# Kernel optimization log

Hardware: AMD Instinct MI355X
Metric: run time of the kernel (lower is better)

The kernel has to match this reference:

```python
import jax, jax.numpy as jnp
import numpy as np

B, T, C, H, W = 16, 32, 64, 16, 16
NUM_FEAT = 10


def setup_inputs() -> dict:
    key = jax.random.key(0)
    ks = jax.random.split(key, 8)
    CHW = C * H * W
    G = NUM_FEAT * H * W
    init = lambda k, shape, fan: jax.random.normal(k, shape, jnp.float32) / np.sqrt(fan).astype(np.float32)
    return {
        "input": jax.random.normal(ks[0], (B, T, C, H, W), jnp.float32),
        "input1": jax.random.normal(ks[1], (B, T, C, H, W), jnp.float32),  # unused by forward
        "act_weights": jax.random.uniform(ks[2], (3,), jnp.float32),
        "conv1_w": init(ks[3], (NUM_FEAT, CHW), CHW),   # Conv1d kernel_size=1 -> plain matmul weight
        "conv1_b": jnp.zeros((NUM_FEAT,), jnp.float32),
        "G3_w": init(ks[4], (G, CHW), CHW),
        "G3_b": jnp.zeros((G,), jnp.float32),
        "ffnn1_w": init(ks[5], (T, T), T),              # torch Linear weight [out,in]
        "ffnn1_b": jnp.zeros((T,), jnp.float32),
    }


def reference(input, input1, act_weights, conv1_w, conv1_b, G3_w, G3_b, ffnn1_w, ffnn1_b):
    Bb, Tt, Cc, Hh, Ww = input.shape
    x = input.reshape(Bb, Tt, Cc * Hh * Ww)                       # [B,T,CHW] (== transposed conv1d input)
    # conv1 (1x1 conv) -> [B,T,F]; AvgPool1d(num_feat) over feature dim -> [B,T]
    f = jnp.einsum('btc,fc->btf', x, conv1_w) + conv1_b
    pooled = f.mean(axis=-1)                                      # [B,T]
    # ffnn1: Linear(T,T): y = pooled @ W^T + b
    z = jnp.einsum('bt,st->bs', pooled, ffnn1_w) + ffnn1_b        # [B,T]
    # G3 (1x1 conv) -> [B,T,G] with G = num_feat*H*W (original permutes to [B,T,G])
    g = jnp.einsum('btc,gc->btg', x, G3_w) + G3_b
    # diag_embed(act(z)) @ g is exactly a per-(b,t) elementwise scale of g.
    gates = (act_weights[0] * jax.nn.relu(z)
             + act_weights[1] * jax.nn.sigmoid(z)
             + act_weights[2] * jax.nn.softmax(z, axis=1))        # softmax over T (dim=1)
    out = (gates[:, :, None] * g).reshape(Bb, Tt, NUM_FEAT, Hh, Ww)
    return out
```

## Files before the change

### kernel.cpp

```cpp
#include <hip/hip_runtime.h>
#include <hip/hip_bf16.h>

#define K_DIM 16384
#define M_DIM 512
#define N_DIM 2560
#define BM 256
#define BN 160
#define BK 64
#define KSPLIT 8
#define KCH (K_DIM / KSPLIT)
#define NT (KCH / BK)

typedef float f32x4 __attribute__((ext_vector_type(4)));
typedef __bf16 bf16x8 __attribute__((ext_vector_type(8)));

__device__ __forceinline__ unsigned short f2bf(float f){
  union { float f; unsigned u; } v; v.f = f;
  unsigned r = v.u + 0x7FFFu + ((v.u >> 16) & 1u);
  return (unsigned short)(r >> 16);
}
__device__ __forceinline__ unsigned bfpack2(float lo, float hi){
  return (unsigned)f2bf(lo) | ((unsigned)f2bf(hi) << 16);
}

__global__ __launch_bounds__(256)
void prep_kernel(const float* __restrict__ conv1_w, const float* __restrict__ conv1_b,
                 float* __restrict__ w_mean, float* __restrict__ b_mean)
{
  int c = blockIdx.x * 256 + threadIdx.x;
  if (c < K_DIM){
    float s = 0.f;
    #pragma unroll
    for (int f = 0; f < 10; ++f) s += conv1_w[f * K_DIM + c];
    w_mean[c] = s * 0.1f;
  }
  if (blockIdx.x == 0 && threadIdx.x == 0){
    float s = 0.f;
    #pragma unroll
    for (int f = 0; f < 10; ++f) s += conv1_b[f];
    *b_mean = s * 0.1f;
  }
}

__global__ __launch_bounds__(256)
void pooled_kernel(const float* __restrict__ X, const float* __restrict__ w_mean,
                   const float* __restrict__ b_mean, float* __restrict__ pooled,
                   unsigned short* __restrict__ xbf)
{
  const int row = blockIdx.x;
  const int tid = threadIdx.x;
  const float* xr = X + (size_t)row * K_DIM;
  unsigned short* xb = xbf + (size_t)row * K_DIM;
  float s = 0.f;
  #pragma unroll 2
  for (int i = 0; i < 8; ++i){
    int idx = (tid + 256 * i) * 8;
    float4 a0 = *(const float4*)(xr + idx);
    float4 a1 = *(const float4*)(xr + idx + 4);
    float4 w0 = *(const float4*)(w_mean + idx);
    float4 w1 = *(const float4*)(w_mean + idx + 4);
    s += a0.x*w0.x + a0.y*w0.y + a0.z*w0.z + a0.w*w0.w
       + a1.x*w1.x + a1.y*w1.y + a1.z*w1.z + a1.w*w1.w;
    uint4 p;
    p.x = bfpack2(a0.x, a0.y); p.y = bfpack2(a0.z, a0.w);
    p.z = bfpack2(a1.x, a1.y); p.w = bfpack2(a1.z, a1.w);
    *(uint4*)(xb + idx) = p;
  }
  #pragma unroll
  for (int off = 32; off; off >>= 1) s += __shfl_down(s, off);
  __shared__ float red[4];
  if ((tid & 63) == 0) red[tid >> 6] = s;
  __syncthreads();
  if (tid == 0) pooled[row] = red[0] + red[1] + red[2] + red[3] + *b_mean;
}

__global__ __launch_bounds__(512)
void gates_kernel(const float* __restrict__ pooled, const float* __restrict__ fw,
                  const float* __restrict__ fb, const float* __restrict__ aw,
                  float* __restrict__ gates)
{
  __shared__ float ps[512];
  int tid = threadIdx.x;
  ps[tid] = pooled[tid];
  __syncthreads();
  int b = tid >> 5, s = tid & 31;
  float z = fb[s];
  #pragma unroll
  for (int t = 0; t < 32; ++t) z += ps[b * 32 + t] * fw[s * 32 + t];
  float mx = z;
  #pragma unroll
  for (int off = 16; off; off >>= 1) mx = fmaxf(mx, __shfl_xor(mx, off));
  float e = expf(z - mx);
  float sum = e;
  #pragma unroll
  for (int off = 16; off; off >>= 1) sum += __shfl_xor(sum, off);
  float sm = e / sum;
  float relu = z > 0.f ? z : 0.f;
  float sig = 1.f / (1.f + expf(-z));
  gates[tid] = aw[0] * relu + aw[1] * sig + aw[2] * sm;
}

__global__ __launch_bounds__(512, 2)
void gemm_kernel(const unsigned short* __restrict__ Abf, const float* __restrict__ W,
                 float* __restrict__ outp, int mode)
{
  __shared__ __align__(16) char smem[106496];
  char* bufA0 = smem;
  char* bufA1 = smem + 32768;
  char* bufB0 = smem + 65536;
  char* bufB1 = smem + 86016;

  const int tid  = threadIdx.x;
  const int lane = tid & 63;
  const int wv   = tid >> 6;
  const int wm   = (wv >> 1) * 64;
  const int wn   = (wv & 1) * 80;

  const int id = blockIdx.x;
  const int kz = id & 7;
  const int r  = id >> 3;
  const int m0 = (r & 1) * BM;
  const int n0 = (r >> 1) * BN;
  const int kbase = kz * KCH;

  f32x4 acc[4][5] = {};

  const int arow0 = tid >> 3;
  const int ac8   = (tid & 7) ^ (arow0 & 7);
  const unsigned short* asrc = Abf + (size_t)(m0 + arow0) * K_DIM + ac8 * 8;
  const int adst = tid * 16;

  auto stageA = [&](char* dst, int k0){
    #pragma unroll
    for (int j = 0; j < 4; ++j){
      __builtin_amdgcn_global_load_lds(
        (const __attribute__((address_space(1))) void*)(asrc + (size_t)j * 64 * K_DIM + k0),
        (__attribute__((address_space(3))) void*)(dst + j * 8192 + adst),
        16, 0, 0);
    }
  };

  const float* bsrcs[5];
  int boff[5];
  #pragma unroll
  for (int j = 0; j < 5; ++j){
    int u = j * 512 + tid;
    int brow = u >> 4;
    int bc4  = u & 15;
    bsrcs[j] = W + (size_t)(n0 + brow) * K_DIM + kbase + bc4 * 4;
    boff[j]  = brow * 128 + ((bc4 * 8) ^ ((brow & 7) << 4));
  }

  auto loadB = [&](int kt, float4* rr){
    #pragma unroll
    for (int j = 0; j < 5; ++j) rr[j] = *(const float4*)(bsrcs[j] + kt * BK);
  };
  auto writeB = [&](char* dst, const float4* rr){
    #pragma unroll
    for (int j = 0; j < 5; ++j){
      uint2 u;
      u.x = bfpack2(rr[j].x, rr[j].y);
      u.y = bfpack2(rr[j].z, rr[j].w);
      *(uint2*)(dst + boff[j]) = u;
    }
  };

  auto compute = [&](const char* A_, const char* B_){
    #pragma unroll
    for (int kk = 0; kk < 2; ++kk){
      bf16x8 af[4], bfv[5];
      const int kbyte = kk * 64 + (lane >> 4) * 16;
      #pragma unroll
      for (int i = 0; i < 4; ++i){
        int row = wm + i * 16 + (lane & 15);
        af[i] = *(const bf16x8*)(A_ + row * 128 + (kbyte ^ ((row & 7) << 4)));
      }
      #pragma unroll
      for (int j = 0; j < 5; ++j){
        int rowb = wn + j * 16 + (lane & 15);
        bfv[j] = *(const bf16x8*)(B_ + rowb * 128 + (kbyte ^ ((rowb & 7) << 4)));
      }
      #pragma unroll
      for (int i = 0; i < 4; ++i)
        #pragma unroll
        for (int j = 0; j < 5; ++j)
          acc[i][j] = __builtin_amdgcn_mfma_f32_16x16x32_bf16(af[i], bfv[j], acc[i][j], 0, 0, 0);
    }
  };

  float4 rbC[5], rbN[5];
  loadB(0, rbC);
  writeB(bufB0, rbC);
  loadB(1, rbC);
  stageA(bufA0, kbase);
  __syncthreads();

  #define BODY(T, RC, RN)                                       \
    do {                                                        \
      char* An = ((T) & 1) ? bufA0 : bufA1;                     \
      char* Ac = ((T) & 1) ? bufA1 : bufA0;                     \
      char* Bc = ((T) & 1) ? bufB1 : bufB0;                     \
      char* Bn = ((T) & 1) ? bufB0 : bufB1;                     \
      if ((T) + 1 < NT) stageA(An, kbase + ((T) + 1) * BK);     \
      if ((T) + 2 < NT) loadB((T) + 2, RN);                     \
      compute(Ac, Bc);                                          \
      __syncthreads();                                          \
      if ((T) + 1 < NT) writeB(Bn, RC);                         \
      __syncthreads();                                          \
    } while (0)

  for (int t = 0; t < NT; t += 2){
    BODY(t, rbC, rbN);
    BODY(t + 1, rbN, rbC);
  }
  #undef BODY

  if (mode == 0){
    float* P = outp + (size_t)kz * M_DIM * N_DIM;
    #pragma unroll
    for (int i = 0; i < 4; ++i){
      int rbase = m0 + wm + i * 16 + (lane >> 4) * 4;
      #pragma unroll
      for (int j = 0; j < 5; ++j){
        int col = n0 + wn + j * 16 + (lane & 15);
        #pragma unroll
        for (int r2 = 0; r2 < 4; ++r2)
          P[(size_t)(rbase + r2) * N_DIM + col] = acc[i][j][r2];
      }
    }
  } else {
    #pragma unroll
    for (int i = 0; i < 4; ++i){
      int rbase = m0 + wm + i * 16 + (lane >> 4) * 4;
      #pragma unroll
      for (int j = 0; j < 5; ++j){
        int col = n0 + wn + j * 16 + (lane & 15);
        #pragma unroll
        for (int r2 = 0; r2 < 4; ++r2)
          atomicAdd(&outp[(size_t)(rbase + r2) * N_DIM + col], acc[i][j][r2]);
      }
    }
  }
}

__global__ __launch_bounds__(256)
void reduce_kernel(const float* __restrict__ part, const float* __restrict__ gates,
                   const float* __restrict__ bias, float* __restrict__ out, int ksplit)
{
  int i4 = blockIdx.x * 256 + threadIdx.x;
  if (i4 >= M_DIM * N_DIM / 4) return;
  size_t off = (size_t)i4 * 4;
  int m = (int)(off / N_DIM);
  int n = (int)(off % N_DIM);
  float sx = 0.f, sy = 0.f, sz = 0.f, sw = 0.f;
  for (int z = 0; z < ksplit; ++z){
    float4 p = *(const float4*)(part + (size_t)z * M_DIM * N_DIM + off);
    sx += p.x; sy += p.y; sz += p.z; sw += p.w;
  }
  float4 bv = *(const float4*)(bias + n);
  float g = gates[m];
  float4 o;
  o.x = g * (sx + bv.x); o.y = g * (sy + bv.y);
  o.z = g * (sz + bv.z); o.w = g * (sw + bv.w);
  *(float4*)(out + off) = o;
}

__global__ __launch_bounds__(256)
void finalize_kernel(float* __restrict__ out, const float* __restrict__ gates,
                     const float* __restrict__ bias)
{
  int i4 = blockIdx.x * 256 + threadIdx.x;
  if (i4 >= M_DIM * N_DIM / 4) return;
  size_t off = (size_t)i4 * 4;
  int m = (int)(off / N_DIM);
  int n = (int)(off % N_DIM);
  float4 o = *(const float4*)(out + off);
  float4 bv = *(const float4*)(bias + n);
  float g = gates[m];
  o.x = g * (o.x + bv.x); o.y = g * (o.y + bv.y);
  o.z = g * (o.z + bv.z); o.w = g * (o.w + bv.w);
  *(float4*)(out + off) = o;
}

extern "C" void kernel_launch(void* const* d_in, const int* in_sizes, int n_in,
                              void* d_out, int out_size, void* d_ws, size_t ws_size,
                              hipStream_t stream)
{
  const float* input   = (const float*)d_in[0];
  const float* aw      = (const float*)d_in[2];
  const float* conv1_w = (const float*)d_in[3];
  const float* conv1_b = (const float*)d_in[4];
  const float* G3_w    = (const float*)d_in[5];
  const float* G3_b    = (const float*)d_in[6];
  const float* ffnn1_w = (const float*)d_in[7];
  const float* ffnn1_b = (const float*)d_in[8];
  float* out = (float*)d_out;

  float* wsf    = (float*)d_ws;
  float* w_mean = wsf;
  float* pooled = wsf + 16384;
  float* gates  = wsf + 16896;
  float* b_mean = wsf + 17408;
  unsigned short* xbf = (unsigned short*)(wsf + 17472);
  float* partial = wsf + 17472 + (size_t)M_DIM * K_DIM / 2;

  const size_t need_det = ((size_t)17472 + (size_t)M_DIM * K_DIM / 2
                           + (size_t)KSPLIT * M_DIM * N_DIM) * 4;

  prep_kernel<<<64, 256, 0, stream>>>(conv1_w, conv1_b, w_mean, b_mean);
  pooled_kernel<<<512, 256, 0, stream>>>(input, w_mean, b_mean, pooled, xbf);
  gates_kernel<<<1, 512, 0, stream>>>(pooled, ffnn1_w, ffnn1_b, aw, gates);

  const int n4 = M_DIM * N_DIM / 4;
  const int grid = (M_DIM / BM) * (N_DIM / BN) * KSPLIT;
  if (ws_size >= need_det){
    gemm_kernel<<<grid, 512, 0, stream>>>(xbf, G3_w, partial, 0);
    reduce_kernel<<<(n4 + 255) / 256, 256, 0, stream>>>(partial, gates, G3_b, out, KSPLIT);
  } else {
    hipMemsetAsync(d_out, 0, (size_t)out_size * sizeof(float), stream);
    gemm_kernel<<<grid, 512, 0, stream>>>(xbf, G3_w, out, 2);
    finalize_kernel<<<(n4 + 255) / 256, 256, 0, stream>>>(out, gates, G3_b);
  }
}
```

Before: 95.87 us.

## Restructure GEMM main loop into single-barrier pipeline with explicit waitcnt

The split-K bf16 GEMM main loop is rebuilt. It now runs one barrier per k-tile instead of two. Both A tiles are prefetched up front through LDS-direct loads, and explicit vmcnt waits let the next A stage and the next B global load stay in flight across the barrier. The B register double-buffer is collapsed to a single set, and the float-to-bf16 packing uses the compiler's native conversion instead of manual rounding. MFMA blocks are wrapped in s_setprio to favour the math wave. The hand-tuned waitcnt values depend on the exact count of issued loads and are fragile if the load counts change.

```diff
diff --git a/kernel.cpp b/kernel.cpp
--- a/kernel.cpp
+++ b/kernel.cpp
@@ -21,6 +21,12 @@
 }
 __device__ __forceinline__ unsigned bfpack2(float lo, float hi){
   return (unsigned)f2bf(lo) | ((unsigned)f2bf(hi) << 16);
+}
+__device__ __forceinline__ unsigned cpk2(float lo, float hi){
+  __bf16 a = (__bf16)lo, b = (__bf16)hi;
+  unsigned short ua = __builtin_bit_cast(unsigned short, a);
+  unsigned short ub = __builtin_bit_cast(unsigned short, b);
+  return (unsigned)ua | ((unsigned)ub << 16);
 }
 
 __global__ __launch_bounds__(256)
@@ -105,10 +111,6 @@
                  float* __restrict__ outp, int mode)
 {
   __shared__ __align__(16) char smem[106496];
-  char* bufA0 = smem;
-  char* bufA1 = smem + 32768;
-  char* bufB0 = smem + 65536;
-  char* bufB1 = smem + 86016;
 
   const int tid  = threadIdx.x;
   const int lane = tid & 63;
@@ -130,7 +132,8 @@
   const unsigned short* asrc = Abf + (size_t)(m0 + arow0) * K_DIM + ac8 * 8;
   const int adst = tid * 16;
 
-  auto stageA = [&](char* dst, int k0){
+  auto stageA = [&](int abuf, int k0){
+    char* dst = smem + (abuf << 15);
     #pragma unroll
     for (int j = 0; j < 4; ++j){
       __builtin_amdgcn_global_load_lds(
@@ -151,21 +154,25 @@
     boff[j]  = brow * 128 + ((bc4 * 8) ^ ((brow & 7) << 4));
   }
 
-  auto loadB = [&](int kt, float4* rr){
-    #pragma unroll
-    for (int j = 0; j < 5; ++j) rr[j] = *(const float4*)(bsrcs[j] + kt * BK);
+  float4 rb[5];
+  auto loadB = [&](int kt){
+    #pragma unroll
+    for (int j = 0; j < 5; ++j) rb[j] = *(const float4*)(bsrcs[j] + kt * BK);
   };
-  auto writeB = [&](char* dst, const float4* rr){
+  auto writeB = [&](int bbuf){
+    char* dst = smem + 65536 + bbuf * 20480;
     #pragma unroll
     for (int j = 0; j < 5; ++j){
       uint2 u;
-      u.x = bfpack2(rr[j].x, rr[j].y);
-      u.y = bfpack2(rr[j].z, rr[j].w);
+      u.x = cpk2(rb[j].x, rb[j].y);
+      u.y = cpk2(rb[j].z, rb[j].w);
       *(uint2*)(dst + boff[j]) = u;
     }
   };
 
-  auto compute = [&](const char* A_, const char* B_){
+  auto compute = [&](int abuf, int bbuf){
+    const char* A_ = smem + (abuf << 15);
+    const char* B_ = smem + 65536 + bbuf * 20480;
     #pragma unroll
     for (int kk = 0; kk < 2; ++kk){
       bf16x8 af[4], bfv[5];
@@ -180,40 +187,35 @@
         int rowb = wn + j * 16 + (lane & 15);
         bfv[j] = *(const bf16x8*)(B_ + rowb * 128 + (kbyte ^ ((rowb & 7) << 4)));
       }
+      __builtin_amdgcn_s_setprio(1);
       #pragma unroll
       for (int i = 0; i < 4; ++i)
         #pragma unroll
         for (int j = 0; j < 5; ++j)
           acc[i][j] = __builtin_amdgcn_mfma_f32_16x16x32_bf16(af[i], bfv[j], acc[i][j], 0, 0, 0);
+      __builtin_amdgcn_s_setprio(0);
     }
   };
 
-  float4 rbC[5], rbN[5];
-  loadB(0, rbC);
-  writeB(bufB0, rbC);
-  loadB(1, rbC);
-  stageA(bufA0, kbase);
-  __syncthreads();
-
-  #define BODY(T, RC, RN)                                       \
-    do {                                                        \
-      char* An = ((T) & 1) ? bufA0 : bufA1;                     \
-      char* Ac = ((T) & 1) ? bufA1 : bufA0;                     \
-      char* Bc = ((T) & 1) ? bufB1 : bufB0;                     \
-      char* Bn = ((T) & 1) ? bufB0 : bufB1;                     \
-      if ((T) + 1 < NT) stageA(An, kbase + ((T) + 1) * BK);     \
-      if ((T) + 2 < NT) loadB((T) + 2, RN);                     \
-      compute(Ac, Bc);                                          \
-      __syncthreads();                                          \
-      if ((T) + 1 < NT) writeB(Bn, RC);                         \
-      __syncthreads();                                          \
-    } while (0)
-
-  for (int t = 0; t < NT; t += 2){
-    BODY(t, rbC, rbN);
-    BODY(t + 1, rbN, rbC);
-  }
-  #undef BODY
+  loadB(0);
+  stageA(0, kbase);
+  writeB(0);
+  loadB(1);
+  stageA(1, kbase + BK);
+  asm volatile("s_waitcnt vmcnt(9) lgkmcnt(0)" ::: "memory");
+  __builtin_amdgcn_s_barrier();
+  __builtin_amdgcn_sched_barrier(0);
+
+  for (int t = 0; t < NT; ++t){
+    writeB((t + 1) & 1);
+    loadB(t + 2 < NT ? t + 2 : NT - 1);
+    compute(t & 1, t & 1);
+    asm volatile("s_waitcnt vmcnt(5) lgkmcnt(0)" ::: "memory");
+    __builtin_amdgcn_s_barrier();
+    __builtin_amdgcn_sched_barrier(0);
+    if (t + 2 < NT)
+      stageA(t & 1, kbase + (t + 2) * BK);
+  }
 
   if (mode == 0){
     float* P = outp + (size_t)kz * M_DIM * N_DIM;
@@ -317,7 +319,7 @@
     gemm_kernel<<<grid, 512, 0, stream>>>(xbf, G3_w, partial, 0);
     reduce_kernel<<<(n4 + 255) / 256, 256, 0, stream>>>(partial, gates, G3_b, out, KSPLIT);
   } else {
-    hipMemsetAsync(d_out, 0, (size_t)out_size * sizeof(float), stream);
+    (void)hipMemsetAsync(d_out, 0, (size_t)out_size * sizeof(float), stream);
     gemm_kernel<<<grid, 512, 0, stream>>>(xbf, G3_w, out, 2);
     finalize_kernel<<<(n4 + 255) / 256, 256, 0, stream>>>(out, gates, G3_b);
   }
```

Measured after the change: 88.12 us. 1.09x faster.
